# Kernel optimization log

Hardware: AMD Instinct MI355X
Metric: run time of the kernel (lower is better)

The kernel has to match this reference:

```python
import jax, jax.numpy as jnp
import numpy as np

B, S, D, H = 8, 1024, 768, 12
DH = D // H  # 64


def setup_inputs() -> dict:
    key = jax.random.key(0)
    ks = jax.random.split(key, 7)
    scale = 0.05
    return {
        "sequences": jax.random.normal(ks[0], (B, S, D), dtype=jnp.float32),
        "Wq": jax.random.normal(ks[1], (H, DH, DH), dtype=jnp.float32) * scale,
        "bq": jax.random.normal(ks[2], (H, DH), dtype=jnp.float32) * scale,
        "Wk": jax.random.normal(ks[3], (H, DH, DH), dtype=jnp.float32) * scale,
        "bk": jax.random.normal(ks[4], (H, DH), dtype=jnp.float32) * scale,
        "Wv": jax.random.normal(ks[5], (H, DH, DH), dtype=jnp.float32) * scale,
        "bv": jax.random.normal(ks[6], (H, DH), dtype=jnp.float32) * scale,
    }


def reference(sequences, Wq, bq, Wk, bk, Wv, bv):
    # sequences: [B, S, D]; per-head slice of width DH gets its own Linear.
    b, s, d = sequences.shape
    h, dh = Wq.shape[0], Wq.shape[-1]
    xh = sequences.reshape(b, s, h, dh)  # [B,S,H,DH] head-chunked features
    q = jnp.einsum('bshd,hde->bshe', xh, Wq) + bq  # [B,S,H,DH]
    k = jnp.einsum('bshd,hde->bshe', xh, Wk) + bk
    v = jnp.einsum('bshd,hde->bshe', xh, Wv) + bv
    scores = jnp.einsum('bqhd,bkhd->bhqk', q, k) / jnp.sqrt(jnp.float32(dh))
    weights = jax.nn.softmax(scores, axis=-1)  # [B,H,S,S]
    out = jnp.einsum('bhqk,bkhd->bqhd', weights, v)  # [B,S,H,DH]
    return out.reshape(b, s, d)  # hstack of heads == reshape back to D
```

## Files before the change

kernel.cpp:

```cpp
#include <hip/hip_runtime.h>
#include <hip/hip_bf16.h>
#include <math.h>

constexpr int Bn = 8, Sn = 1024, Dn = 768, Hn = 12, DHn = 64;
constexpr int QKV_ELEMS = Bn * Hn * Sn * DHn;
constexpr float SQC = 0.42466086f;

typedef __attribute__((ext_vector_type(8))) short bf16x8;
typedef __attribute__((ext_vector_type(4))) float f32x4;

__device__ __forceinline__ unsigned int pk2bf(float a, float b) {
    union { __hip_bfloat162 h; unsigned u; } r;
    r.h = __float22bfloat162_rn(make_float2(a, b));
    return r.u;
}

__device__ __forceinline__ void quad_net(unsigned &X, unsigned &Y, int quad) {
    unsigned v = (quad >= 2) ? X : Y;
    v = __shfl_xor(v, 32, 64);
    unsigned X1 = (quad >= 2) ? v : X;
    unsigned Y1 = (quad >= 2) ? Y : v;
    unsigned w2 = (quad & 1) ? X1 : Y1;
    w2 = __shfl_xor(w2, 16, 64);
    X = (quad & 1) ? w2 : X1;
    Y = (quad & 1) ? Y1 : w2;
}

__device__ __forceinline__ bf16x8 wfrag(const float* __restrict__ W,
                                        int e, int kc, int quad, float sc) {
    const float* p = W + (size_t)(kc * 32 + quad * 8) * 64 + e;
    unsigned int tmp[4];
    #pragma unroll
    for (int j = 0; j < 4; j++)
        tmp[j] = pk2bf(p[(2 * j) * 64] * sc, p[(2 * j + 1) * 64] * sc);
    return *(bf16x8*)tmp;
}

__global__ __launch_bounds__(256) void proj_kernel(
    const float* __restrict__ x,
    const float* __restrict__ Wk, const float* __restrict__ bk,
    const float* __restrict__ Wv, const float* __restrict__ bv,
    unsigned short* __restrict__ k_ws, unsigned short* __restrict__ vt_ws)
{
    __shared__ unsigned short Xs[64 * 72];
    __shared__ unsigned short ObK[64 * 72];
    __shared__ unsigned short ObV[64 * 72];

    const int blk  = blockIdx.x;
    const int xcd  = blk & 7;
    const int g    = blk >> 3;
    const int bh   = xcd * 12 + (g % 12);
    const int tile = g / 12;
    const int h    = bh % Hn;
    const int b    = bh / Hn;
    const int t    = threadIdx.x;
    const int w    = t >> 6;
    const int lane = t & 63;
    const int l    = lane & 15;
    const int quad = lane >> 4;
    const int sr   = t >> 2;
    const int sc0  = (t & 3) * 16;
    const int s0   = tile * 64;

    {
        const float* xrow = x + ((size_t)(b * Sn + s0 + sr) * Dn + h * 64 + sc0);
        unsigned int tmp[8];
        #pragma unroll
        for (int q4 = 0; q4 < 4; q4++) {
            float4 v = ((const float4*)xrow)[q4];
            tmp[2 * q4 + 0] = pk2bf(v.x, v.y);
            tmp[2 * q4 + 1] = pk2bf(v.z, v.w);
        }
        *(uint4*)&Xs[sr * 72 + sc0]     = ((uint4*)tmp)[0];
        *(uint4*)&Xs[sr * 72 + sc0 + 8] = ((uint4*)tmp)[1];
    }

    const int e = w * 16 + l;
    bf16x8 wk[2], wv[2];
    #pragma unroll
    for (int kc = 0; kc < 2; kc++) {
        wk[kc] = wfrag(Wk + (size_t)h * 4096, e, kc, quad, SQC);
        wv[kc] = wfrag(Wv + (size_t)h * 4096, e, kc, quad, 1.0f);
    }
    float4 bkv = *(const float4*)(bk + h * 64 + w * 16 + quad * 4);
    bkv.x *= SQC; bkv.y *= SQC; bkv.z *= SQC; bkv.w *= SQC;
    const float bvl = bv[h * 64 + e];

    __syncthreads();

    bf16x8 xf[4][2];
    #pragma unroll
    for (int nt = 0; nt < 4; nt++)
        #pragma unroll
        for (int kc = 0; kc < 2; kc++)
            xf[nt][kc] = *(bf16x8*)&Xs[(nt * 16 + l) * 72 + kc * 32 + quad * 8];

    #pragma unroll
    for (int nt = 0; nt < 4; nt++) {
        f32x4 ak = (f32x4){bkv.x, bkv.y, bkv.z, bkv.w};
        ak = __builtin_amdgcn_mfma_f32_16x16x32_bf16(wk[0], xf[nt][0], ak, 0, 0, 0);
        ak = __builtin_amdgcn_mfma_f32_16x16x32_bf16(wk[1], xf[nt][1], ak, 0, 0, 0);
        *(uint2*)&ObK[(nt * 16 + l) * 72 + w * 16 + quad * 4] =
            make_uint2(pk2bf(ak[0], ak[1]), pk2bf(ak[2], ak[3]));
        f32x4 av = (f32x4){bvl, bvl, bvl, bvl};
        av = __builtin_amdgcn_mfma_f32_16x16x32_bf16(xf[nt][0], wv[0], av, 0, 0, 0);
        av = __builtin_amdgcn_mfma_f32_16x16x32_bf16(xf[nt][1], wv[1], av, 0, 0, 0);
        *(uint2*)&ObV[(w * 16 + l) * 72 + nt * 16 + quad * 4] =
            make_uint2(pk2bf(av[0], av[1]), pk2bf(av[2], av[3]));
    }
    __syncthreads();

    {
        uint4 a  = *(uint4*)&ObK[sr * 72 + sc0];
        uint4 b4 = *(uint4*)&ObK[sr * 72 + sc0 + 8];
        unsigned short* dst = k_ws + (size_t)(bh * Sn + s0 + sr) * 64 + sc0;
        ((uint4*)dst)[0] = a;
        *(uint4*)(dst + 8) = b4;
    }
    {
        uint4 a  = *(uint4*)&ObV[sr * 72 + sc0];
        uint4 b4 = *(uint4*)&ObV[sr * 72 + sc0 + 8];
        unsigned short* dst = vt_ws + (size_t)bh * 64 * Sn + (size_t)sr * Sn + s0 + sc0;
        ((uint4*)dst)[0] = a;
        *(uint4*)(dst + 8) = b4;
    }
}

__global__ __launch_bounds__(256, 3) void attn_kernel(
    const float* __restrict__ x,
    const float* __restrict__ Wq, const float* __restrict__ bq,
    const unsigned short* __restrict__ k_ws,
    const unsigned short* __restrict__ vt_ws,
    float* __restrict__ out)
{
    __shared__ unsigned short Ks[2][64 * 72];
    __shared__ unsigned short Vt[2][64 * 72];

    const int blk = blockIdx.x;
    const int xcd = blk & 7;
    const int idx = blk >> 3;
    const int bh  = xcd * 12 + (idx % 12);
    const int qt  = idx / 12;
    const int t    = threadIdx.x;
    const int w    = t >> 6;
    const int lane = t & 63;
    const int l    = lane & 15;
    const int quad = lane >> 4;
    const int sr   = t >> 2;
    const int sc0  = (t & 3) * 16;

    const int b = bh / Hn, h = bh % Hn;
    const size_t base  = (size_t)bh * Sn * 64;
    const size_t vbase = (size_t)bh * 64 * Sn;

    bf16x8 qf[2][2];
    {
        bf16x8 xq[2][2];
        #pragma unroll
        for (int st = 0; st < 2; st++) {
            const float* xp = x + ((size_t)(b * Sn + qt * 128 + w * 32 + st * 16 + l) * Dn
                                   + h * 64 + quad * 8);
            #pragma unroll
            for (int kc = 0; kc < 2; kc++) {
                float4 v0 = *(const float4*)(xp + kc * 32);
                float4 v1 = *(const float4*)(xp + kc * 32 + 4);
                unsigned int tmp[4] = {pk2bf(v0.x, v0.y), pk2bf(v0.z, v0.w),
                                       pk2bf(v1.x, v1.y), pk2bf(v1.z, v1.w)};
                xq[st][kc] = *(bf16x8*)tmp;
            }
        }
        unsigned qq[2][4][2];
        #pragma unroll
        for (int nt = 0; nt < 4; nt++) {
            bf16x8 wa0 = wfrag(Wq + (size_t)h * 4096, nt * 16 + l, 0, quad, SQC);
            bf16x8 wa1 = wfrag(Wq + (size_t)h * 4096, nt * 16 + l, 1, quad, SQC);
            float4 bqv = *(const float4*)(bq + h * 64 + nt * 16 + quad * 4);
            #pragma unroll
            for (int st = 0; st < 2; st++) {
                f32x4 acc = (f32x4){bqv.x * SQC, bqv.y * SQC, bqv.z * SQC, bqv.w * SQC};
                acc = __builtin_amdgcn_mfma_f32_16x16x32_bf16(wa0, xq[st][0], acc, 0, 0, 0);
                acc = __builtin_amdgcn_mfma_f32_16x16x32_bf16(wa1, xq[st][1], acc, 0, 0, 0);
                qq[st][nt][0] = pk2bf(acc[0], acc[1]);
                qq[st][nt][1] = pk2bf(acc[2], acc[3]);
            }
        }
        #pragma unroll
        for (int st = 0; st < 2; st++)
            #pragma unroll
            for (int kc = 0; kc < 2; kc++) {
                unsigned t0 = qq[st][2 * kc][0], u0 = qq[st][2 * kc + 1][0];
                unsigned t1 = qq[st][2 * kc][1], u1 = qq[st][2 * kc + 1][1];
                quad_net(t0, u0, quad);
                quad_net(t1, u1, quad);
                unsigned tmp[4] = {t0, t1, u0, u1};
                qf[st][kc] = *(bf16x8*)tmp;
            }
    }

    f32x4 Oa[2][4];
    #pragma unroll
    for (int st = 0; st < 2; st++)
        #pragma unroll
        for (int nt = 0; nt < 4; nt++) Oa[st][nt] = (f32x4){0.f, 0.f, 0.f, 0.f};
    float ps[2] = {0.f, 0.f};

    const unsigned short* kpp = k_ws + base + (size_t)sr * 64 + sc0;
    const unsigned short* vpp = vt_ws + vbase + (size_t)sr * Sn + sc0;
    uint4 kpre0 = ((const uint4*)kpp)[0];
    uint4 kpre1 = ((const uint4*)(kpp + 8))[0];
    uint4 vpre0 = ((const uint4*)vpp)[0];
    uint4 vpre1 = ((const uint4*)(vpp + 8))[0];

    for (int kt = 0; kt < 16; kt++) {
        unsigned short* KsC = Ks[kt & 1];
        unsigned short* VtC = Vt[kt & 1];
        {
            *(uint4*)&KsC[sr * 72 + sc0]     = kpre0;
            *(uint4*)&KsC[sr * 72 + sc0 + 8] = kpre1;
            *(uint4*)&VtC[sr * 72 + sc0]     = vpre0;
            *(uint4*)&VtC[sr * 72 + sc0 + 8] = vpre1;
        }
        __syncthreads();

        if (kt + 1 < 16) {
            kpp += 64 * 64;
            vpp += 64;
            kpre0 = ((const uint4*)kpp)[0];
            kpre1 = ((const uint4*)(kpp + 8))[0];
            vpre0 = ((const uint4*)vpp)[0];
            vpre1 = ((const uint4*)(vpp + 8))[0];
        }

        unsigned pp[2][4][2];
        #pragma unroll
        for (int nt = 0; nt < 4; nt++) {
            bf16x8 kf0 = *(bf16x8*)&KsC[(nt * 16 + l) * 72 + quad * 8];
            bf16x8 kf1 = *(bf16x8*)&KsC[(nt * 16 + l) * 72 + 32 + quad * 8];
            #pragma unroll
            for (int st = 0; st < 2; st++) {
                f32x4 s = (f32x4){0.f, 0.f, 0.f, 0.f};
                s = __builtin_amdgcn_mfma_f32_16x16x32_bf16(kf0, qf[st][0], s, 0, 0, 0);
                s = __builtin_amdgcn_mfma_f32_16x16x32_bf16(kf1, qf[st][1], s, 0, 0, 0);
                float p0 = exp2f(s[0]), p1 = exp2f(s[1]);
                float p2 = exp2f(s[2]), p3 = exp2f(s[3]);
                ps[st] += (p0 + p1) + (p2 + p3);
                pp[st][nt][0] = pk2bf(p0, p1);
                pp[st][nt][1] = pk2bf(p2, p3);
            }
        }

        bf16x8 pb[2][2];
        #pragma unroll
        for (int st = 0; st < 2; st++)
            #pragma unroll
            for (int kc = 0; kc < 2; kc++) {
                unsigned t0 = pp[st][2 * kc][0], u0 = pp[st][2 * kc + 1][0];
                unsigned t1 = pp[st][2 * kc][1], u1 = pp[st][2 * kc + 1][1];
                quad_net(t0, u0, quad);
                quad_net(t1, u1, quad);
                unsigned tmp[4] = {t0, t1, u0, u1};
                pb[st][kc] = *(bf16x8*)tmp;
            }

        #pragma unroll
        for (int nt = 0; nt < 4; nt++) {
            bf16x8 vf0 = *(bf16x8*)&VtC[(nt * 16 + l) * 72 + quad * 8];
            bf16x8 vf1 = *(bf16x8*)&VtC[(nt * 16 + l) * 72 + 32 + quad * 8];
            #pragma unroll
            for (int st = 0; st < 2; st++) {
                Oa[st][nt] = __builtin_amdgcn_mfma_f32_16x16x32_bf16(vf0, pb[st][0], Oa[st][nt], 0, 0, 0);
                Oa[st][nt] = __builtin_amdgcn_mfma_f32_16x16x32_bf16(vf1, pb[st][1], Oa[st][nt], 0, 0, 0);
            }
        }
    }

    #pragma unroll
    for (int st = 0; st < 2; st++) {
        ps[st] += __shfl_xor(ps[st], 16, 64);
        ps[st] += __shfl_xor(ps[st], 32, 64);
        const float inv = 1.0f / ps[st];
        const int srow = qt * 128 + w * 32 + st * 16 + l;
        #pragma unroll
        for (int nt = 0; nt < 4; nt++) {
            float4 o = make_float4(Oa[st][nt][0] * inv, Oa[st][nt][1] * inv,
                                   Oa[st][nt][2] * inv, Oa[st][nt][3] * inv);
            *(float4*)&out[(size_t)(b * Sn + srow) * Dn + h * 64 + nt * 16 + quad * 4] = o;
        }
    }
}

extern "C" void kernel_launch(void* const* d_in, const int* in_sizes, int n_in,
                              void* d_out, int out_size, void* d_ws, size_t ws_size,
                              hipStream_t stream) {
    const float* x  = (const float*)d_in[0];
    const float* Wq = (const float*)d_in[1];
    const float* bq = (const float*)d_in[2];
    const float* Wk = (const float*)d_in[3];
    const float* bk = (const float*)d_in[4];
    const float* Wv = (const float*)d_in[5];
    const float* bv = (const float*)d_in[6];
    float* out = (float*)d_out;

    unsigned short* k_ws  = (unsigned short*)d_ws;
    unsigned short* vt_ws = k_ws + QKV_ELEMS;

    hipLaunchKernelGGL(proj_kernel, dim3(Bn * Hn * 16), dim3(256), 0, stream,
                       x, Wk, bk, Wv, bv, k_ws, vt_ws);
    hipLaunchKernelGGL(attn_kernel, dim3(Bn * Hn * 8), dim3(256), 0, stream,
                       x, Wq, bq, k_ws, vt_ws, out);
}
```

Before: 149.8 us.

## Split key dimension across two wave groups per block with LDS reduction

The attention block doubles to 512 threads. Two groups of four waves each process half of the key sequence, 512 keys in 8 tiles, for the same 128 queries. At the end the partial outputs and softmax sums are combined through LDS. This halves the serial loop length per wave and raises the wave count to hide latency. In exchange it drops the LDS double buffering, so each iteration needs an extra barrier, and it adds a final reduction step. The code relies on softmax without max subtraction, which makes the partial sums directly additive.

Result: slower. 326.8 us (+118.2%).

```diff
diff --git a/kernel.cpp b/kernel.cpp
--- a/kernel.cpp
+++ b/kernel.cpp
@@ -126,15 +126,15 @@
     }
 }
 
-__global__ __launch_bounds__(256, 3) void attn_kernel(
+__global__ __launch_bounds__(512, 6) void attn_kernel(
     const float* __restrict__ x,
     const float* __restrict__ Wq, const float* __restrict__ bq,
     const unsigned short* __restrict__ k_ws,
     const unsigned short* __restrict__ vt_ws,
     float* __restrict__ out)
 {
-    __shared__ unsigned short Ks[2][64 * 72];
-    __shared__ unsigned short Vt[2][64 * 72];
+    __shared__ unsigned short SMEM[4 * 64 * 72];
+    __shared__ float cPs[2 * 256];
 
     const int blk = blockIdx.x;
     const int xcd = blk & 7;
@@ -143,22 +143,27 @@
     const int qt  = idx / 12;
     const int t    = threadIdx.x;
     const int w    = t >> 6;
+    const int wq   = w & 3;
+    const int grp  = w >> 2;
     const int lane = t & 63;
     const int l    = lane & 15;
     const int quad = lane >> 4;
-    const int sr   = t >> 2;
-    const int sc0  = (t & 3) * 16;
+    const int tl   = t & 255;
+    const int sr   = tl >> 2;
+    const int sc0  = (tl & 3) * 16;
 
     const int b = bh / Hn, h = bh % Hn;
     const size_t base  = (size_t)bh * Sn * 64;
     const size_t vbase = (size_t)bh * 64 * Sn;
+    unsigned short* Ksg = SMEM + grp * 4608;
+    unsigned short* Vtg = SMEM + 9216 + grp * 4608;
 
     bf16x8 qf[2][2];
     {
         bf16x8 xq[2][2];
         #pragma unroll
         for (int st = 0; st < 2; st++) {
-            const float* xp = x + ((size_t)(b * Sn + qt * 128 + w * 32 + st * 16 + l) * Dn
+            const float* xp = x + ((size_t)(b * Sn + qt * 128 + wq * 32 + st * 16 + l) * Dn
                                    + h * 64 + quad * 8);
             #pragma unroll
             for (int kc = 0; kc < 2; kc++) {
@@ -204,25 +209,24 @@
         for (int nt = 0; nt < 4; nt++) Oa[st][nt] = (f32x4){0.f, 0.f, 0.f, 0.f};
     float ps[2] = {0.f, 0.f};
 
-    const unsigned short* kpp = k_ws + base + (size_t)sr * 64 + sc0;
-    const unsigned short* vpp = vt_ws + vbase + (size_t)sr * Sn + sc0;
+    const unsigned short* kpp = k_ws + base + (size_t)(grp * 512 + sr) * 64 + sc0;
+    const unsigned short* vpp = vt_ws + vbase + (size_t)sr * Sn + grp * 512 + sc0;
     uint4 kpre0 = ((const uint4*)kpp)[0];
     uint4 kpre1 = ((const uint4*)(kpp + 8))[0];
     uint4 vpre0 = ((const uint4*)vpp)[0];
     uint4 vpre1 = ((const uint4*)(vpp + 8))[0];
 
-    for (int kt = 0; kt < 16; kt++) {
-        unsigned short* KsC = Ks[kt & 1];
-        unsigned short* VtC = Vt[kt & 1];
+    for (int kt = 0; kt < 8; kt++) {
+        __syncthreads();
         {
-            *(uint4*)&KsC[sr * 72 + sc0]     = kpre0;
-            *(uint4*)&KsC[sr * 72 + sc0 + 8] = kpre1;
-            *(uint4*)&VtC[sr * 72 + sc0]     = vpre0;
-            *(uint4*)&VtC[sr * 72 + sc0 + 8] = vpre1;
+            *(uint4*)&Ksg[sr * 72 + sc0]     = kpre0;
+            *(uint4*)&Ksg[sr * 72 + sc0 + 8] = kpre1;
+            *(uint4*)&Vtg[sr * 72 + sc0]     = vpre0;
+            *(uint4*)&Vtg[sr * 72 + sc0 + 8] = vpre1;
         }
         __syncthreads();
 
-        if (kt + 1 < 16) {
+        if (kt + 1 < 8) {
             kpp += 64 * 64;
             vpp += 64;
             kpre0 = ((const uint4*)kpp)[0];
@@ -234,8 +238,8 @@
         unsigned pp[2][4][2];
         #pragma unroll
         for (int nt = 0; nt < 4; nt++) {
-            bf16x8 kf0 = *(bf16x8*)&KsC[(nt * 16 + l) * 72 + quad * 8];
-            bf16x8 kf1 = *(bf16x8*)&KsC[(nt * 16 + l) * 72 + 32 + quad * 8];
+            bf16x8 kf0 = *(bf16x8*)&Ksg[(nt * 16 + l) * 72 + quad * 8];
+            bf16x8 kf1 = *(bf16x8*)&Ksg[(nt * 16 + l) * 72 + 32 + quad * 8];
             #pragma unroll
             for (int st = 0; st < 2; st++) {
                 f32x4 s = (f32x4){0.f, 0.f, 0.f, 0.f};
@@ -264,8 +268,8 @@
 
         #pragma unroll
         for (int nt = 0; nt < 4; nt++) {
-            bf16x8 vf0 = *(bf16x8*)&VtC[(nt * 16 + l) * 72 + quad * 8];
-            bf16x8 vf1 = *(bf16x8*)&VtC[(nt * 16 + l) * 72 + 32 + quad * 8];
+            bf16x8 vf0 = *(bf16x8*)&Vtg[(nt * 16 + l) * 72 + quad * 8];
+            bf16x8 vf1 = *(bf16x8*)&Vtg[(nt * 16 + l) * 72 + 32 + quad * 8];
             #pragma unroll
             for (int st = 0; st < 2; st++) {
                 Oa[st][nt] = __builtin_amdgcn_mfma_f32_16x16x32_bf16(vf0, pb[st][0], Oa[st][nt], 0, 0, 0);
@@ -278,13 +282,36 @@
     for (int st = 0; st < 2; st++) {
         ps[st] += __shfl_xor(ps[st], 16, 64);
         ps[st] += __shfl_xor(ps[st], 32, 64);
-        const float inv = 1.0f / ps[st];
-        const int srow = qt * 128 + w * 32 + st * 16 + l;
-        #pragma unroll
-        for (int nt = 0; nt < 4; nt++) {
-            float4 o = make_float4(Oa[st][nt][0] * inv, Oa[st][nt][1] * inv,
-                                   Oa[st][nt][2] * inv, Oa[st][nt][3] * inv);
-            *(float4*)&out[(size_t)(b * Sn + srow) * Dn + h * 64 + nt * 16 + quad * 4] = o;
+    }
+
+    float* cO = (float*)SMEM;
+    const int li = wq * 64 + lane;
+    __syncthreads();
+    if (grp == 1) {
+        #pragma unroll
+        for (int st = 0; st < 2; st++) {
+            #pragma unroll
+            for (int nt = 0; nt < 4; nt++)
+                *(f32x4*)&cO[(st * 4 + nt) * 1024 + li * 4] = Oa[st][nt];
+            cPs[st * 256 + li] = ps[st];
+        }
+    }
+    __syncthreads();
+    if (grp == 0) {
+        #pragma unroll
+        for (int st = 0; st < 2; st++) {
+            ps[st] += cPs[st * 256 + li];
+            const float inv = 1.0f / ps[st];
+            const int srow = qt * 128 + wq * 32 + st * 16 + l;
+            #pragma unroll
+            for (int nt = 0; nt < 4; nt++) {
+                f32x4 o2 = *(f32x4*)&cO[(st * 4 + nt) * 1024 + li * 4];
+                float4 o = make_float4((Oa[st][nt][0] + o2[0]) * inv,
+                                       (Oa[st][nt][1] + o2[1]) * inv,
+                                       (Oa[st][nt][2] + o2[2]) * inv,
+                                       (Oa[st][nt][3] + o2[3]) * inv);
+                *(float4*)&out[(size_t)(b * Sn + srow) * Dn + h * 64 + nt * 16 + quad * 4] = o;
+            }
         }
     }
 }
@@ -306,6 +333,6 @@
 
     hipLaunchKernelGGL(proj_kernel, dim3(Bn * Hn * 16), dim3(256), 0, stream,
                        x, Wk, bk, Wv, bv, k_ws, vt_ws);
-    hipLaunchKernelGGL(attn_kernel, dim3(Bn * Hn * 8), dim3(256), 0, stream,
+    hipLaunchKernelGGL(attn_kernel, dim3(Bn * Hn * 8), dim3(512), 0, stream,
                        x, Wq, bq, k_ws, vt_ws, out);
 }
```
